# Performance work log

Measured on AMD Instinct MI355X. Metric: run time of the kernel, lower is better.

Reference implementation:

```python
import jax, jax.numpy as jnp
import numpy as np
from jax import lax

HEATMAP_THRESH = 0.1


def _conv(x, w, b, stride=1):
    y = lax.conv_general_dilated(x, w, (stride, stride), 'SAME',
                                 dimension_numbers=('NCHW', 'OIHW', 'NCHW'))
    return y + b[None, :, None, None]


def _maxpool2(x):
    return lax.reduce_window(x, -jnp.inf, lax.max, (1, 1, 2, 2), (1, 1, 2, 2), 'VALID')


def _up2(x):
    return jnp.repeat(jnp.repeat(x, 2, axis=2), 2, axis=3)


def _find_peaks_mask(hm, thresh):
    # Vectorized equivalent of the CPU nested-loop _find_peaks:
    # interior pixel is a peak iff v > thresh and v >= its 4 axial neighbors.
    c = hm[:, :, 1:-1, 1:-1]
    m = ((c > thresh)
         & (c >= hm[:, :, :-2, 1:-1]) & (c >= hm[:, :, 2:, 1:-1])
         & (c >= hm[:, :, 1:-1, :-2]) & (c >= hm[:, :, 1:-1, 2:]))
    return jnp.pad(m, ((0, 0), (0, 0), (1, 1), (1, 1)))  # border never a peak


def _param(key, shape):
    fan_in = int(np.prod(shape[1:]))
    return jax.random.normal(key, shape, jnp.float32) / np.sqrt(fan_in)


_SHAPES = {
    'w_d1': (32, 3, 3, 3), 'w_d2': (64, 32, 3, 3), 'w_bn': (128, 64, 3, 3),
    'w_u1': (64, 192, 3, 3), 'w_u2': (32, 96, 3, 3), 'w_seg': (1, 32, 1, 1),
    'w_p1': (64, 4, 3, 3), 'w_p2': (128, 64, 3, 3),
    'w_hm': (17, 128, 1, 1), 'w_paf': (32, 128, 1, 1),
}


def setup_inputs() -> dict:
    key = jax.random.key(0)
    ks = jax.random.split(key, 1 + len(_SHAPES))
    B, H, W = 8, 384, 384
    inp = {'x': jax.random.normal(ks[0], (B, 3, H, W), jnp.float32)}
    for i, (n, s) in enumerate(_SHAPES.items()):
        inp[n] = _param(ks[i + 1], s)
        inp[n.replace('w_', 'b_')] = jnp.zeros((s[0],), jnp.float32)
    return inp


def _forward(x, w_d1, b_d1, w_d2, b_d2, w_bn, b_bn, w_u1, b_u1, w_u2, b_u2,
             w_seg, b_seg, w_p1, b_p1, w_p2, b_p2, w_hm, b_hm, w_paf, b_paf):
    # --- UNet segmentation ---
    d1 = jax.nn.relu(_conv(x, w_d1, b_d1))                    # [B,32,384,384]
    d2 = jax.nn.relu(_conv(_maxpool2(d1), w_d2, b_d2))        # [B,64,192,192]
    bn = jax.nn.relu(_conv(_maxpool2(d2), w_bn, b_bn))        # [B,128,96,96]
    u1 = jax.nn.relu(_conv(jnp.concatenate([_up2(bn), d2], 1), w_u1, b_u1))  # [B,64,192,192]
    u2 = jax.nn.relu(_conv(jnp.concatenate([_up2(u1), d1], 1), w_u2, b_u2))  # [B,32,384,384]
    seg = _conv(u2, w_seg, b_seg)                             # [B,1,384,384]
    # --- Pose net on image + detached seg logits ---
    xp = jnp.concatenate([x, lax.stop_gradient(seg)], axis=1)  # detach()
    p1 = jax.nn.relu(_conv(xp, w_p1, b_p1, stride=2))          # [B,64,192,192]
    p2 = jax.nn.relu(_conv(p1, w_p2, b_p2, stride=2))          # [B,128,96,96]
    hm = _conv(p2, w_hm, b_hm)                                 # [B,17,96,96]
    paf = _conv(p2, w_paf, b_paf)                              # [B,32,96,96]
    return seg, hm, paf


def reference(x, w_d1, b_d1, w_d2, b_d2, w_bn, b_bn, w_u1, b_u1, w_u2, b_u2,
              w_seg, b_seg, w_p1, b_p1, w_p2, b_p2, w_hm, b_hm, w_paf, b_paf):
    seg, hm, paf = _forward(x, w_d1, b_d1, w_d2, b_d2, w_bn, b_bn, w_u1, b_u1,
                            w_u2, b_u2, w_seg, b_seg, w_p1, b_p1, w_p2, b_p2,
                            w_hm, b_hm, w_paf, b_paf)
    # jit-friendly replacement for the variable-length python peak lists:
    # boolean mask over [B,K,h,w]; (x,y) coords recoverable via jnp.nonzero offline.
    peaks = _find_peaks_mask(hm, HEATMAP_THRESH)
    return seg, hm, paf, peaks
```

## Files before the change

### kernel.cpp

```cpp
#include <hip/hip_runtime.h>


#define BS 256
#define BSW 512

typedef _Float16 half8 __attribute__((ext_vector_type(8)));
typedef float floatx4 __attribute__((ext_vector_type(4)));

#define LDSDW 20
#define PLT8 10000
#define ESTR 388

__global__ __launch_bounds__(BS) void packw_gen_kernel(
    const float* __restrict__ w, _Float16* __restrict__ bp, int Cin, int Cout)
{
    int total = (Cin >> 5) * 9 * (Cout >> 4) * 64;
    int tid = blockIdx.x * BS + threadIdx.x;
    if (tid >= total) return;
    int lane = tid & 63;
    int t = tid >> 6;
    int NTl = Cout >> 4;
    int nt = t % NTl; t /= NTl;
    int tap = t % 9;
    int chunk = t / 9;
    int q = lane >> 4, n = lane & 15;
    int co = nt * 16 + n;
    _Float16* ph = bp + (size_t)tid * 8;
    _Float16* pl = bp + (size_t)total * 8 + (size_t)tid * 8;
#pragma unroll
    for (int j = 0; j < 8; ++j) {
        int ci = chunk * 32 + q * 8 + j;
        float v = w[((size_t)co * Cin + ci) * 9 + tap];
        _Float16 h = (_Float16)v;
        ph[j] = h;
        pl[j] = (_Float16)(v - (float)h);
    }
}

__global__ __launch_bounds__(BS) void packw_1x1_kernel(
    const float* __restrict__ w, _Float16* __restrict__ bp, int Cin, int NTl, int Cout)
{
    int total = (Cin >> 5) * NTl * 64;
    int tid = blockIdx.x * BS + threadIdx.x;
    if (tid >= total) return;
    int lane = tid & 63;
    int t = tid >> 6;
    int nt = t % NTl;
    int chunk = t / NTl;
    int q = lane >> 4, n = lane & 15;
    int co = nt * 16 + n;
    _Float16* ph = bp + (size_t)tid * 8;
    _Float16* pl = bp + (size_t)total * 8 + (size_t)tid * 8;
#pragma unroll
    for (int j = 0; j < 8; ++j) {
        int ci = chunk * 32 + q * 8 + j;
        float v = (co < Cout) ? w[(size_t)co * Cin + ci] : 0.f;
        _Float16 h = (_Float16)v;
        ph[j] = h;
        pl[j] = (_Float16)(v - (float)h);
    }
}

template <int TCO>
__global__ __launch_bounds__(BS, 2) void conv3x3_pool_kernel(
    const float* __restrict__ inA, int Ca,
    const float* __restrict__ w, const float* __restrict__ b,
    _Float16* __restrict__ oph, _Float16* __restrict__ opl,
    int N, int H, int W, int Cout)
{
    const int W8 = W >> 3;
    const int H2 = H >> 1, W2 = W >> 1;
    int idx = blockIdx.x * BS + threadIdx.x;
    int total = N * H2 * W8;
    if (idx >= total) return;
    int x8 = idx % W8;
    int t  = idx / W8;
    int yo = t % H2;
    int n  = t / H2;
    int x0 = x8 << 3;
    const int co0 = blockIdx.y * TCO;
    const bool left_ok  = (x0 > 0);
    const bool right_ok = (x0 + 8 < W);
    const int Cin = Ca;

    float pool[TCO][4];

#pragma unroll
    for (int rr = 0; rr < 2; ++rr) {
        int y = 2 * yo + rr;
        float acc[TCO][8];
#pragma unroll
        for (int j = 0; j < TCO; ++j) {
            float bv = b[co0 + j];
#pragma unroll
            for (int p = 0; p < 8; ++p) acc[j][p] = bv;
        }

        for (int ci = 0; ci < Cin; ++ci) {
            float v[3][10];
#pragma unroll
            for (int ky = 0; ky < 3; ++ky) {
                int iy = y + ky - 1;
                if (iy < 0 || iy >= H) {
#pragma unroll
                    for (int p = 0; p < 10; ++p) v[ky][p] = 0.f;
                    continue;
                }
                const float* r = inA + ((size_t)(n * Ca + ci) * H + iy) * W;
                v[ky][0] = left_ok ? r[x0 - 1] : 0.f;
                float4 q0 = *(const float4*)(r + x0);
                float4 q1 = *(const float4*)(r + x0 + 4);
                v[ky][1] = q0.x; v[ky][2] = q0.y; v[ky][3] = q0.z; v[ky][4] = q0.w;
                v[ky][5] = q1.x; v[ky][6] = q1.y; v[ky][7] = q1.z; v[ky][8] = q1.w;
                v[ky][9] = right_ok ? r[x0 + 8] : 0.f;
            }
#pragma unroll
            for (int j = 0; j < TCO; ++j) {
                const float* wp = w + ((size_t)(co0 + j) * Cin + ci) * 9;
#pragma unroll
                for (int ky = 0; ky < 3; ++ky) {
                    float w0 = wp[ky * 3 + 0], w1 = wp[ky * 3 + 1], w2 = wp[ky * 3 + 2];
#pragma unroll
                    for (int p = 0; p < 8; ++p)
                        acc[j][p] += w0 * v[ky][p] + w1 * v[ky][p + 1] + w2 * v[ky][p + 2];
                }
            }
        }

#pragma unroll
        for (int j = 0; j < TCO; ++j) {
#pragma unroll
            for (int p4 = 0; p4 < 4; ++p4) {
                float mrow = fmaxf(fmaxf(acc[j][2 * p4], 0.f),
                                   fmaxf(acc[j][2 * p4 + 1], 0.f));
                pool[j][p4] = (rr == 0) ? mrow : fmaxf(pool[j][p4], mrow);
            }
        }
    }

#pragma unroll
    for (int p4 = 0; p4 < 4; ++p4) {
        half8 hv, lv;
#pragma unroll
        for (int j = 0; j < 8; ++j) {
            float v = pool[j][p4];
            _Float16 hh = (_Float16)v;
            hv[j] = hh;
            lv[j] = (_Float16)(v - (float)hh);
        }
        size_t oa = ((size_t)((n * (Cout >> 3) + (co0 >> 3)) * H2 + yo) * W2
                     + (x0 >> 1) + p4) * 8;
        *(half8*)(oph + oa) = hv;
        *(half8*)(opl + oa) = lv;
    }
}

template <int CHUNKS, int NT, int HH, int WW, int OUTMODE>
__global__ __launch_bounds__(BS) void conv3x3s_mfma_kernel(
    const _Float16* __restrict__ inh, const _Float16* __restrict__ inl,
    const _Float16* __restrict__ bp,
    const float* __restrict__ bias,
    float* __restrict__ out,
    _Float16* __restrict__ osph,
    _Float16* __restrict__ ospl,
    _Float16* __restrict__ oph,
    _Float16* __restrict__ opl)
{
    constexpr int PL = 4 * 34 * LDSDW;
    constexpr int EPI = 64 * NT * 16;
    constexpr int LDS_DW = (2 * PL > EPI) ? 2 * PL : EPI;
    __shared__ unsigned int lds[LDS_DW];

    int xblks = WW / 32;
    int b = blockIdx.x;
    int xb = b % xblks; b /= xblks;
    int yp = b % (HH / 2);
    int n  = b / (HH / 2);
    int y0 = yp * 2;
    int x0 = xb * 32;

    int tid = threadIdx.x;
    int lane = tid & 63, wv = tid >> 6;
    int m = lane & 15, q = lane >> 4;
    int lrow = wv >> 1;
    int lx   = (wv & 1) * 16;

    floatx4 acc[NT];
#pragma unroll
    for (int nt = 0; nt < NT; ++nt) acc[nt] = (floatx4){0.f, 0.f, 0.f, 0.f};

    const int planeW = CHUNKS * 9 * NT * 64 * 8;

    for (int chunk = 0; chunk < CHUNKS; ++chunk) {
        __syncthreads();
        for (int e = tid; e < 4 * 34 * 4; e += BS) {
            int xi = e % 34;
            int rest = e / 34;
            int oct = rest & 3;
            int row = rest >> 2;
            int iy = y0 - 1 + row, gx = x0 - 1 + xi;
            half8 hv = {}, lv = {};
            if (iy >= 0 && iy < HH && gx >= 0 && gx < WW) {
                size_t ga = ((size_t)((n * (CHUNKS * 4) + chunk * 4 + oct) * HH + iy) * WW + gx) * 8;
                hv = *(const half8*)(inh + ga);
                lv = *(const half8*)(inl + ga);
            }
            int base = (row * 34 + xi) * LDSDW + oct * 4;
            *(half8*)((char*)lds + (size_t)base * 4) = hv;
            *(half8*)((char*)lds + ((size_t)PL + base) * 4) = lv;
        }
        __syncthreads();
#pragma unroll
        for (int ky = 0; ky < 3; ++ky) {
#pragma unroll
            for (int kx = 0; kx < 3; ++kx) {
                int row = lrow + ky;
                int xi  = lx + m + kx;
                int adw = (row * 34 + xi) * LDSDW + q * 4;
                half8 ah = *(const half8*)((const char*)lds + (size_t)adw * 4);
                half8 al = *(const half8*)((const char*)lds + ((size_t)PL + adw) * 4);
                int tap = ky * 3 + kx;
                const _Float16* bpp = bp + ((size_t)(chunk * 9 + tap) * NT) * 64 * 8;
#pragma unroll
                for (int nt = 0; nt < NT; ++nt) {
                    half8 bh = *(const half8*)(bpp + ((size_t)nt * 64 + lane) * 8);
                    half8 bl = *(const half8*)(bpp + planeW + ((size_t)nt * 64 + lane) * 8);
                    acc[nt] = __builtin_amdgcn_mfma_f32_16x16x32_f16(ah, bh, acc[nt], 0, 0, 0);
                    acc[nt] = __builtin_amdgcn_mfma_f32_16x16x32_f16(ah, bl, acc[nt], 0, 0, 0);
                    acc[nt] = __builtin_amdgcn_mfma_f32_16x16x32_f16(al, bh, acc[nt], 0, 0, 0);
                }
            }
        }
    }

    __syncthreads();
#pragma unroll
    for (int nt = 0; nt < NT; ++nt) {
#pragma unroll
        for (int r = 0; r < 4; ++r) {
            int co = nt * 16 + m;
            int pxl = wv * 16 + q * 4 + r;
            ((float*)lds)[co * 64 + pxl] = acc[nt][r];
        }
    }
    __syncthreads();
    if (OUTMODE == 0 || OUTMODE == 2) {
        constexpr int thPerCo = 256 / (NT * 16);
        constexpr int pxPerTh = 64 / thPerCo;
        int co = tid / thPerCo;
        int sub = tid % thPerCo;
        int pxb = sub * pxPerTh;
        float bb = bias[co];
#pragma unroll
        for (int u = 0; u < pxPerTh; u += 4) {
            int p = pxb + u;
            int row = y0 + (p >> 5), xx = x0 + (p & 31);
            const float* lp = (const float*)lds + co * 64 + p;
            float4 vv = *(const float4*)lp;
            vv.x = fmaxf(vv.x + bb, 0.f);
            vv.y = fmaxf(vv.y + bb, 0.f);
            vv.z = fmaxf(vv.z + bb, 0.f);
            vv.w = fmaxf(vv.w + bb, 0.f);
            *(float4*)(out + ((size_t)(n * NT * 16 + co) * HH + row) * WW + xx) = vv;
        }
    }
    if (OUTMODE >= 1) {
        constexpr int OCTS = NT * 2;
        for (int it = tid; it < OCTS * 64; it += BS) {
            int px = it & 63;
            int oct = it >> 6;
            int row = y0 + (px >> 5), xx = x0 + (px & 31);
            half8 hv, lv;
#pragma unroll
            for (int j = 0; j < 8; ++j) {
                float v = fmaxf(((float*)lds)[(oct * 8 + j) * 64 + px] + bias[oct * 8 + j], 0.f);
                _Float16 hh = (_Float16)v;
                hv[j] = hh;
                lv[j] = (_Float16)(v - (float)hh);
            }
            size_t oaddr = ((size_t)((n * OCTS + oct) * HH + row) * WW + xx) * 8;
            *(half8*)(osph + oaddr) = hv;
            *(half8*)(ospl + oaddr) = lv;
        }
    }
    if (OUTMODE == 3) {
        constexpr int OCTS = NT * 2;
        constexpr int HHo = HH / 2, WWo = WW / 2;
        for (int it = tid; it < OCTS * 16; it += BS) {
            int xo = it & 15;
            int oct = it >> 4;
            half8 hv, lv;
#pragma unroll
            for (int j = 0; j < 8; ++j) {
                const float* base = (const float*)lds + (oct * 8 + j) * 64;
                float bb = bias[oct * 8 + j];
                float t0 = fmaxf(fmaxf(base[2 * xo] + bb, 0.f),
                                 fmaxf(base[2 * xo + 1] + bb, 0.f));
                float t1 = fmaxf(fmaxf(base[32 + 2 * xo] + bb, 0.f),
                                 fmaxf(base[32 + 2 * xo + 1] + bb, 0.f));
                float v = fmaxf(t0, t1);
                _Float16 hh = (_Float16)v;
                hv[j] = hh;
                lv[j] = (_Float16)(v - (float)hh);
            }
            size_t oaddr = ((size_t)((n * OCTS + oct) * HHo + yp) * WWo + (x0 >> 1) + xo) * 8;
            *(half8*)(oph + oaddr) = hv;
            *(half8*)(opl + oaddr) = lv;
        }
    }
}

template <int CHUNKS, int NT, int WI>
__global__ __launch_bounds__(BS) void conv3x3s2s_mfma_kernel(
    const _Float16* __restrict__ inh, const _Float16* __restrict__ inl,
    const _Float16* __restrict__ bp,
    const float* __restrict__ bias,
    _Float16* __restrict__ oh, _Float16* __restrict__ ol_)
{
    constexpr int WO = WI / 2;
    constexpr int PLs = 5 * 68 * LDSDW;
    constexpr int EPI = 64 * NT * 16;
    constexpr int LDS_DW = (2 * PLs > EPI) ? 2 * PLs : EPI;
    __shared__ unsigned int lds[LDS_DW];

    int xblks = WO / 32;
    int b = blockIdx.x;
    int xb = b % xblks; b /= xblks;
    int yp = b % (WO / 2);
    int n  = b / (WO / 2);
    int y0 = yp * 2;
    int x0 = xb * 32;

    int tid = threadIdx.x;
    int lane = tid & 63, wv = tid >> 6;
    int m = lane & 15, q = lane >> 4;
    int lrow = wv >> 1;
    int lx   = (wv & 1) * 16;

    floatx4 acc[NT];
#pragma unroll
    for (int nt = 0; nt < NT; ++nt) acc[nt] = (floatx4){0.f, 0.f, 0.f, 0.f};

    const int planeW = CHUNKS * 9 * NT * 64 * 8;

    for (int chunk = 0; chunk < CHUNKS; ++chunk) {
        __syncthreads();
        for (int e = tid; e < 5 * 68 * 4; e += BS) {
            int xi = e % 68;
            int rest = e / 68;
            int oct = rest & 3;
            int row = rest >> 2;
            int iy = 2 * y0 + row, ix = 2 * x0 + xi;
            half8 hv = {}, lv = {};
            if (xi < 65 && iy < WI && ix < WI) {
                size_t ga = ((size_t)((n * (CHUNKS * 4) + chunk * 4 + oct) * WI + iy) * WI + ix) * 8;
                hv = *(const half8*)(inh + ga);
                lv = *(const half8*)(inl + ga);
            }
            int pos = (xi & 1) * 34 + (xi >> 1);
            int base = (row * 68 + pos) * LDSDW + oct * 4;
            *(half8*)((char*)lds + (size_t)base * 4) = hv;
            *(half8*)((char*)lds + ((size_t)PLs + base) * 4) = lv;
        }
        __syncthreads();
#pragma unroll
        for (int ky = 0; ky < 3; ++ky) {
#pragma unroll
            for (int kx = 0; kx < 3; ++kx) {
                int row = 2 * lrow + ky;
                int pos = (kx & 1) * 34 + (lx + m) + (kx >> 1);
                int adw = (row * 68 + pos) * LDSDW + q * 4;
                half8 ah = *(const half8*)((const char*)lds + (size_t)adw * 4);
                half8 al = *(const half8*)((const char*)lds + ((size_t)PLs + adw) * 4);
                int tap = ky * 3 + kx;
                const _Float16* bpp = bp + ((size_t)(chunk * 9 + tap) * NT) * 64 * 8;
#pragma unroll
                for (int nt = 0; nt < NT; ++nt) {
                    half8 bh = *(const half8*)(bpp + ((size_t)nt * 64 + lane) * 8);
                    half8 bl = *(const half8*)(bpp + planeW + ((size_t)nt * 64 + lane) * 8);
                    acc[nt] = __builtin_amdgcn_mfma_f32_16x16x32_f16(ah, bh, acc[nt], 0, 0, 0);
                    acc[nt] = __builtin_amdgcn_mfma_f32_16x16x32_f16(ah, bl, acc[nt], 0, 0, 0);
                    acc[nt] = __builtin_amdgcn_mfma_f32_16x16x32_f16(al, bh, acc[nt], 0, 0, 0);
                }
            }
        }
    }

    __syncthreads();
#pragma unroll
    for (int nt = 0; nt < NT; ++nt) {
#pragma unroll
        for (int r = 0; r < 4; ++r) {
            int co = nt * 16 + m;
            int pxl = wv * 16 + q * 4 + r;
            ((float*)lds)[co * 64 + pxl] = acc[nt][r];
        }
    }
    __syncthreads();
    {
        constexpr int OCTS = NT * 2;
        for (int it = tid; it < OCTS * 64; it += BS) {
            int px = it & 63;
            int oct = it >> 6;
            int row = y0 + (px >> 5), xx = x0 + (px & 31);
            half8 hv, lv;
#pragma unroll
            for (int j = 0; j < 8; ++j) {
                float v = fmaxf(((float*)lds)[(oct * 8 + j) * 64 + px] + bias[oct * 8 + j], 0.f);
                _Float16 hh = (_Float16)v;
                hv[j] = hh;
                lv[j] = (_Float16)(v - (float)hh);
            }
            size_t oaddr = ((size_t)((n * OCTS + oct) * WO + row) * WO + xx) * 8;
            *(half8*)(oh + oaddr) = hv;
            *(half8*)(ol_ + oaddr) = lv;
        }
    }
}

template <int CHUNKS, int NT>
__global__ __launch_bounds__(BS) void conv1x1s_mfma_kernel(
    const _Float16* __restrict__ inh, const _Float16* __restrict__ inl,
    const _Float16* __restrict__ bp,
    const float* __restrict__ bias,
    float* __restrict__ out,
    int Cout, int HW)
{
    constexpr int PL1 = 64 * LDSDW;
    constexpr int EPI = 64 * NT * 16;
    constexpr int LDS_DW = (2 * PL1 > EPI) ? 2 * PL1 : EPI;
    __shared__ unsigned int lds[LDS_DW];

    int pblks = HW / 64;
    int b = blockIdx.x;
    int pb = b % pblks;
    int n  = b / pblks;
    int sp0 = pb * 64;

    int tid = threadIdx.x;
    int lane = tid & 63, wv = tid >> 6;
    int m = lane & 15, q = lane >> 4;

    floatx4 acc[NT];
#pragma unroll
    for (int nt = 0; nt < NT; ++nt) acc[nt] = (floatx4){0.f, 0.f, 0.f, 0.f};

    const int planeW = CHUNKS * NT * 64 * 8;

    for (int chunk = 0; chunk < CHUNKS; ++chunk) {
        __syncthreads();
        {
            int px = tid & 63;
            int oct = tid >> 6;
            size_t ga = (((size_t)(n * (CHUNKS * 4) + chunk * 4 + oct)) * HW + sp0 + px) * 8;
            half8 hv = *(const half8*)(inh + ga);
            half8 lv = *(const half8*)(inl + ga);
            int base = px * LDSDW + oct * 4;
            *(half8*)((char*)lds + (size_t)base * 4) = hv;
            *(half8*)((char*)lds + ((size_t)PL1 + base) * 4) = lv;
        }
        __syncthreads();
        {
            int adw = (wv * 16 + m) * LDSDW + q * 4;
            half8 ah = *(const half8*)((const char*)lds + (size_t)adw * 4);
            half8 al = *(const half8*)((const char*)lds + ((size_t)PL1 + adw) * 4);
            const _Float16* bpp = bp + ((size_t)chunk * NT) * 64 * 8;
#pragma unroll
            for (int nt = 0; nt < NT; ++nt) {
                half8 bh = *(const half8*)(bpp + ((size_t)nt * 64 + lane) * 8);
                half8 bl = *(const half8*)(bpp + planeW + ((size_t)nt * 64 + lane) * 8);
                acc[nt] = __builtin_amdgcn_mfma_f32_16x16x32_f16(ah, bh, acc[nt], 0, 0, 0);
                acc[nt] = __builtin_amdgcn_mfma_f32_16x16x32_f16(ah, bl, acc[nt], 0, 0, 0);
                acc[nt] = __builtin_amdgcn_mfma_f32_16x16x32_f16(al, bh, acc[nt], 0, 0, 0);
            }
        }
    }

    __syncthreads();
#pragma unroll
    for (int nt = 0; nt < NT; ++nt) {
#pragma unroll
        for (int r = 0; r < 4; ++r) {
            ((float*)lds)[(nt * 16 + m) * 64 + wv * 16 + q * 4 + r] = acc[nt][r];
        }
    }
    __syncthreads();
    {
        constexpr int thPerCo = 256 / (NT * 16);
        constexpr int pxPerTh = 64 / thPerCo;
        int co = tid / thPerCo;
        int g  = tid % thPerCo;
        if (co < Cout) {
            float bb = bias[co];
            const float* lp = (const float*)lds + co * 64 + g * pxPerTh;
            float* op = out + ((size_t)(n * Cout + co)) * HW + sp0 + g * pxPerTh;
#pragma unroll
            for (int u = 0; u < pxPerTh; u += 4) {
                float4 vv = *(const float4*)(lp + u);
                vv.x += bb; vv.y += bb; vv.z += bb; vv.w += bb;
                *(float4*)(op + u) = vv;
            }
        }
    }
}

__global__ __launch_bounds__(BSW) void u1_mfma_kernel(
    const _Float16* __restrict__ bnh, const _Float16* __restrict__ bnl,
    const _Float16* __restrict__ d2h, const _Float16* __restrict__ d2l,
    const _Float16* __restrict__ bp,
    const float* __restrict__ b_u1,
    _Float16* __restrict__ oh, _Float16* __restrict__ ol_)
{
    __shared__ unsigned int lds[2 * PLT8];
    const int Ho = 192, Wo = 192;
    int b = blockIdx.x;
    int xb = b % 4; b /= 4;
    int yb = b % 24;
    int n  = b / 24;
    int y0 = yb * 8;
    int x0 = xb * 48;

    int tid = threadIdx.x;
    int lane = tid & 63, wv = tid >> 6;
    int m = lane & 15, q = lane >> 4;
    int yr = y0 + wv;

    floatx4 acc[3][4];
#pragma unroll
    for (int mt = 0; mt < 3; ++mt)
#pragma unroll
        for (int nt = 0; nt < 4; ++nt) acc[mt][nt] = (floatx4){0.f, 0.f, 0.f, 0.f};

    const int hh0 = (y0 - 1) >> 1;
    const int hx0 = (x0 - 1) >> 1;

    for (int chunk = 0; chunk < 6; ++chunk) {
        __syncthreads();
        if (chunk < 4) {
            for (int e = tid; e < 6 * 26 * 4; e += BSW) {
                int xi = e % 26;
                int rest = e / 26;
                int oct = rest & 3;
                int row = rest >> 2;
                int hy = hh0 + row, hx = hx0 + xi;
                half8 hv = {}, lv = {};
                if (hy >= 0 && hy < 96 && hx >= 0 && hx < 96) {
                    size_t ga = ((size_t)((n * 16 + chunk * 4 + oct) * 96 + hy) * 96 + hx) * 8;
                    hv = *(const half8*)(bnh + ga);
                    lv = *(const half8*)(bnl + ga);
                }
                int base = (row * 50 + xi) * LDSDW + oct * 4;
                *(half8*)((char*)lds + (size_t)base * 4) = hv;
                *(half8*)((char*)lds + ((size_t)PLT8 + base) * 4) = lv;
            }
        } else {
            for (int e = tid; e < 10 * 50 * 4; e += BSW) {
                int xi = e % 50;
                int rest = e / 50;
                int oct = rest & 3;
                int row = rest >> 2;
                int iy = y0 - 1 + row, gx = x0 - 1 + xi;
                half8 hv = {}, lv = {};
                if (iy >= 0 && iy < Ho && gx >= 0 && gx < Wo) {
                    size_t ga = ((size_t)((n * 8 + (chunk - 4) * 4 + oct) * Ho + iy) * Wo + gx) * 8;
                    hv = *(const half8*)(d2h + ga);
                    lv = *(const half8*)(d2l + ga);
                }
                int base = (row * 50 + xi) * LDSDW + oct * 4;
                *(half8*)((char*)lds + (size_t)base * 4) = hv;
                *(half8*)((char*)lds + ((size_t)PLT8 + base) * 4) = lv;
            }
        }
        __syncthreads();
#pragma unroll
        for (int ky = 0; ky < 3; ++ky) {
#pragma unroll
            for (int kx = 0; kx < 3; ++kx) {
                int tap = ky * 3 + kx;
                const _Float16* bpp = bp + ((size_t)(chunk * 9 + tap) * 4) * 64 * 8;
                half8 bh[4], bl[4];
#pragma unroll
                for (int nt = 0; nt < 4; ++nt) {
                    bh[nt] = *(const half8*)(bpp + ((size_t)nt * 64 + lane) * 8);
                    bl[nt] = *(const half8*)(bpp + 110592 + ((size_t)nt * 64 + lane) * 8);
                }
                int row;
                if (chunk < 4) row = ((yr + ky - 1) >> 1) - hh0;
                else           row = wv + ky;
#pragma unroll
                for (int mt = 0; mt < 3; ++mt) {
                    int px = 16 * mt + m;
                    int xi = (chunk < 4) ? (((x0 + px + kx - 1) >> 1) - hx0)
                                         : (px + kx);
                    int adw = (row * 50 + xi) * LDSDW + q * 4;
                    half8 ah = *(const half8*)((const char*)lds + (size_t)adw * 4);
                    half8 al = *(const half8*)((const char*)lds + ((size_t)PLT8 + adw) * 4);
#pragma unroll
                    for (int nt = 0; nt < 4; ++nt) {
                        acc[mt][nt] = __builtin_amdgcn_mfma_f32_16x16x32_f16(ah, bh[nt], acc[mt][nt], 0, 0, 0);
                        acc[mt][nt] = __builtin_amdgcn_mfma_f32_16x16x32_f16(ah, bl[nt], acc[mt][nt], 0, 0, 0);
                        acc[mt][nt] = __builtin_amdgcn_mfma_f32_16x16x32_f16(al, bh[nt], acc[mt][nt], 0, 0, 0);
                    }
                }
            }
        }
    }

#pragma unroll
    for (int h = 0; h < 2; ++h) {
        __syncthreads();
#pragma unroll
        for (int ntl = 0; ntl < 2; ++ntl) {
#pragma unroll
            for (int mt = 0; mt < 3; ++mt) {
#pragma unroll
                for (int r = 0; r < 4; ++r) {
                    ((float*)lds)[(ntl * 16 + m) * ESTR + wv * 48 + 16 * mt + q * 4 + r]
                        = acc[mt][h * 2 + ntl][r];
                }
            }
        }
        __syncthreads();
        for (int it = tid; it < 4 * 384; it += BSW) {
            int px = it % 384;
            int ol = it / 384;
            int row = y0 + px / 48, xx = x0 + px % 48;
            half8 hv, lv;
#pragma unroll
            for (int j = 0; j < 8; ++j) {
                int col = ol * 8 + j;
                float v = fmaxf(((float*)lds)[col * ESTR + px] + b_u1[h * 32 + col], 0.f);
                _Float16 hh = (_Float16)v;
                hv[j] = hh;
                lv[j] = (_Float16)(v - (float)hh);
            }
            size_t oaddr = ((size_t)((n * 8 + h * 4 + ol) * Ho + row) * Wo + xx) * 8;
            *(half8*)(oh + oaddr) = hv;
            *(half8*)(ol_ + oaddr) = lv;
        }
    }
}

__global__ __launch_bounds__(BSW) void u2seg_mfma_kernel(
    const _Float16* __restrict__ u1h, const _Float16* __restrict__ u1l,
    const _Float16* __restrict__ d1h, const _Float16* __restrict__ d1l,
    const _Float16* __restrict__ bp,
    const float* __restrict__ b_u2,
    const float* __restrict__ w_seg,
    const float* __restrict__ b_seg,
    float* __restrict__ seg)
// ... 244 lines not shown
    int n  = t / Ho;
    int ox0 = q << 2;
    int ix0 = ox0 << 1;
    const int co0 = blockIdx.y * TCO;
    const bool right_ok = (ix0 + 8 < Wi);
    const int Cin = Ca + Cb;

    float acc[TCO][4];
#pragma unroll
    for (int j = 0; j < TCO; ++j) {
        float bv = b[co0 + j];
        acc[j][0] = bv; acc[j][1] = bv; acc[j][2] = bv; acc[j][3] = bv;
    }

    for (int ci = 0; ci < Cin; ++ci) {
        const float* base = (ci < Ca)
            ? inA + (size_t)(n * Ca + ci) * Hi * Wi
            : inB + (size_t)(n * Cb + (ci - Ca)) * Hi * Wi;
        float v[3][9];
#pragma unroll
        for (int ky = 0; ky < 3; ++ky) {
            int iy = 2 * oy + ky;
            if (iy >= Hi) {
#pragma unroll
                for (int p = 0; p < 9; ++p) v[ky][p] = 0.f;
                continue;
            }
            const float* r = base + (size_t)iy * Wi + ix0;
            float4 a = *(const float4*)r;
            float4 c = *(const float4*)(r + 4);
            v[ky][0] = a.x; v[ky][1] = a.y; v[ky][2] = a.z; v[ky][3] = a.w;
            v[ky][4] = c.x; v[ky][5] = c.y; v[ky][6] = c.z; v[ky][7] = c.w;
            v[ky][8] = right_ok ? r[8] : 0.f;
        }
#pragma unroll
        for (int j = 0; j < TCO; ++j) {
            const float* wp = w + ((size_t)(co0 + j) * Cin + ci) * 9;
#pragma unroll
            for (int ky = 0; ky < 3; ++ky) {
                float w0 = wp[ky * 3 + 0], w1 = wp[ky * 3 + 1], w2 = wp[ky * 3 + 2];
#pragma unroll
                for (int p = 0; p < 4; ++p)
                    acc[j][p] += w0 * v[ky][2 * p] + w1 * v[ky][2 * p + 1] + w2 * v[ky][2 * p + 2];
            }
        }
    }

    if (SPLIT) {
#pragma unroll
        for (int p = 0; p < 4; ++p) {
            half8 hv, lv;
#pragma unroll
            for (int j = 0; j < 8; ++j) {
                float v = acc[j][p];
                if (do_relu) v = fmaxf(v, 0.f);
                _Float16 hh = (_Float16)v;
                hv[j] = hh;
                lv[j] = (_Float16)(v - (float)hh);
            }
            size_t oaddr = ((size_t)((n * (Cout >> 3) + (co0 >> 3)) * Ho + oy) * Wo + ox0 + p) * 8;
            *(half8*)(osph + oaddr) = hv;
            *(half8*)(ospl + oaddr) = lv;
        }
    } else {
#pragma unroll
        for (int j = 0; j < TCO; ++j) {
            float4 o;
            o.x = acc[j][0]; o.y = acc[j][1]; o.z = acc[j][2]; o.w = acc[j][3];
            if (do_relu) {
                o.x = fmaxf(o.x, 0.f); o.y = fmaxf(o.y, 0.f);
                o.z = fmaxf(o.z, 0.f); o.w = fmaxf(o.w, 0.f);
            }
            *(float4*)(out + ((size_t)(n * Cout + co0 + j) * Ho + oy) * Wo + ox0) = o;
        }
    }
}

__global__ __launch_bounds__(BS) void peaks_kernel(
    const float* __restrict__ hm, float* __restrict__ out,
    int NC, int H, int W, float thresh)
{
    int idx = blockIdx.x * BS + threadIdx.x;
    int total = NC * H * W;
    if (idx >= total) return;
    int x = idx % W;
    int t = idx / W;
    int y = t % H;
    int c = t / H;
    float r = 0.f;
    if (x >= 1 && x < W - 1 && y >= 1 && y < H - 1) {
        const float* base = hm + (size_t)c * H * W;
        float cv = base[y * W + x];
        if (cv > thresh &&
            cv >= base[(y - 1) * W + x] &&
            cv >= base[(y + 1) * W + x] &&
            cv >= base[y * W + (x - 1)] &&
            cv >= base[y * W + (x + 1)])
            r = 1.f;
    }
    out[idx] = r;
}

static inline int nblk(long n) { return (int)((n + BS - 1) / BS); }

extern "C" void kernel_launch(void* const* d_in, const int* in_sizes, int n_in,
                              void* d_out, int out_size, void* d_ws, size_t ws_size,
                              hipStream_t stream)
{
    const float* x     = (const float*)d_in[0];
    const float* w_d1  = (const float*)d_in[1];  const float* b_d1  = (const float*)d_in[2];
    const float* w_d2  = (const float*)d_in[3];  const float* b_d2  = (const float*)d_in[4];
    const float* w_bn  = (const float*)d_in[5];  const float* b_bn  = (const float*)d_in[6];
    const float* w_u1  = (const float*)d_in[7];  const float* b_u1  = (const float*)d_in[8];
    const float* w_u2  = (const float*)d_in[9];  const float* b_u2  = (const float*)d_in[10];
    const float* w_seg = (const float*)d_in[11]; const float* b_seg = (const float*)d_in[12];
    const float* w_p1  = (const float*)d_in[13]; const float* b_p1  = (const float*)d_in[14];
    const float* w_p2  = (const float*)d_in[15]; const float* b_p2  = (const float*)d_in[16];
    const float* w_hm  = (const float*)d_in[17]; const float* b_hm  = (const float*)d_in[18];
    const float* w_paf = (const float*)d_in[19]; const float* b_paf = (const float*)d_in[20];

    const int N = 8, H = 384, W = 384;
    const int H2 = 192, W2 = 192, H4 = 96, W4 = 96;

    float* ws = (float*)d_ws;
    _Float16* pd1sp_h = (_Float16*)(ws);
    _Float16* pd1sp_l = (_Float16*)(ws + 4718592);
    _Float16* d2sp_h = (_Float16*)(ws + 28311552);
    _Float16* d2sp_l = (_Float16*)(ws + 37748736);
    _Float16* pd2sp_h = (_Float16*)(ws + 47185920);
    _Float16* pd2sp_l = (_Float16*)(ws + 49545216);
    _Float16* bnsp_h = (_Float16*)(ws + 18874368);
    _Float16* bnsp_l = (_Float16*)(ws + 23592960);
    _Float16* u1sp_h = (_Float16*)(ws);
    _Float16* u1sp_l = (_Float16*)(ws + 9437184);
    _Float16* d1sp_h = (_Float16*)(ws + 18874368);
    _Float16* d1sp_l = (_Float16*)(ws + 37748736);
    _Float16* p1sp_h = (_Float16*)(ws);
    _Float16* p1sp_l = (_Float16*)(ws + 9437184);
    _Float16* p2sp_h = (_Float16*)(ws + 18874368);
    _Float16* p2sp_l = (_Float16*)(ws + 23592960);

    float* out_seg   = (float*)d_out;
    float* out_hm    = out_seg + 1179648;
    float* out_paf   = out_hm + 1253376;
    float* out_peaks = out_paf + 2359296;
    _Float16* bp_u1  = (_Float16*)(out_seg + 4792320);
    _Float16* bp_u2  = (_Float16*)(out_seg + 4902912);
    _Float16* bp_d2  = (_Float16*)(out_seg + 4930560);
    _Float16* bp_bn  = (_Float16*)(out_seg + 4948992);
    _Float16* bp_p2  = (_Float16*)(out_seg + 5022720);
    _Float16* bp_hm  = (_Float16*)(out_seg + 5096448);
    _Float16* bp_paf = (_Float16*)(out_seg + 5100544);

    packw_gen_kernel<<<nblk(13824), BS, 0, stream>>>(w_u1, bp_u1, 192, 64);
    packw_gen_kernel<<<nblk(3456),  BS, 0, stream>>>(w_u2, bp_u2, 96, 32);
    packw_gen_kernel<<<nblk(2304),  BS, 0, stream>>>(w_d2, bp_d2, 32, 64);
    packw_gen_kernel<<<nblk(9216),  BS, 0, stream>>>(w_bn, bp_bn, 64, 128);
    packw_gen_kernel<<<nblk(9216),  BS, 0, stream>>>(w_p2, bp_p2, 64, 128);
    packw_1x1_kernel<<<nblk(512),   BS, 0, stream>>>(w_hm, bp_hm, 128, 2, 17);
    packw_1x1_kernel<<<nblk(512),   BS, 0, stream>>>(w_paf, bp_paf, 128, 2, 32);
    {
        dim3 g(nblk((long)N * H2 * (W / 8)), 32 / 8);
        conv3x3_pool_kernel<8><<<g, BS, 0, stream>>>(
            x, 3, w_d1, b_d1, pd1sp_h, pd1sp_l, N, H, W, 32);
    }
    conv3x3s_mfma_kernel<1, 4, 192, 192, 3><<<8 * 96 * 6, BS, 0, stream>>>(
        pd1sp_h, pd1sp_l, bp_d2, b_d2, nullptr, d2sp_h, d2sp_l, pd2sp_h, pd2sp_l);
    conv3x3s_mfma_kernel<2, 8, 96, 96, 1><<<8 * 48 * 3, BS, 0, stream>>>(
        pd2sp_h, pd2sp_l, bp_bn, b_bn, nullptr, bnsp_h, bnsp_l, nullptr, nullptr);
    u1_mfma_kernel<<<8 * 24 * 4, BSW, 0, stream>>>(
        bnsp_h, bnsp_l, d2sp_h, d2sp_l, bp_u1, b_u1, u1sp_h, u1sp_l);
    {
        dim3 g(nblk((long)N * H * (W / 8)), 32 / 8);
        conv3x3_x8_kernel<1, 8, 1><<<g, BS, 0, stream>>>(
            x, 3, nullptr, 0, w_d1, b_d1, nullptr, N, H, W, 32, 1, d1sp_h, d1sp_l);
    }
    u2seg_mfma_kernel<<<8 * 48 * 8, BSW, 0, stream>>>(
        u1sp_h, u1sp_l, d1sp_h, d1sp_l, bp_u2, b_u2, w_seg, b_seg, out_seg);
    {
        dim3 g(nblk((long)N * H2 * (W2 / 4)), 64 / 8);
        conv3x3_s2_co_kernel<8, 1><<<g, BS, 0, stream>>>(
            x, 3, out_seg, 1, w_p1, b_p1, nullptr, N, H, W, 64, 1, p1sp_h, p1sp_l);
    }
    conv3x3s2s_mfma_kernel<2, 8, 192><<<8 * 48 * 3, BS, 0, stream>>>(
        p1sp_h, p1sp_l, bp_p2, b_p2, p2sp_h, p2sp_l);
    conv1x1s_mfma_kernel<4, 2><<<8 * 144, BS, 0, stream>>>(
        p2sp_h, p2sp_l, bp_hm, b_hm, out_hm, 17, H4 * W4);
    conv1x1s_mfma_kernel<4, 2><<<8 * 144, BS, 0, stream>>>(
        p2sp_h, p2sp_l, bp_paf, b_paf, out_paf, 32, H4 * W4);
    peaks_kernel<<<nblk((long)N * 17 * H4 * W4), BS, 0, stream>>>(
        out_hm, out_peaks, N * 17, H4, W4, 0.1f);
}
```

Before: 906.5 us.

## Merge weight-pack launches, fuse 1x1 heads, retile d2 conv to 8-row blocks

Replaces seven weight-packing launches with one combined kernel, and fuses the heatmap and PAF 1x1 convolutions into a single kernel that reads p2 once. Adds a dedicated d2 conv kernel using 512-thread blocks over 8x48 tiles with 3x4 MFMA accumulators, which also writes the pooled output. The goal is to cut launch overhead, avoid reading p2 twice, and improve reuse of LDS input and weights. The cost is higher register pressure and a two-pass epilogue in the new d2 kernel.

```diff
diff --git a/kernel.cpp b/kernel.cpp
--- a/kernel.cpp
+++ b/kernel.cpp
@@ -11,12 +11,10 @@
 #define PLT8 10000
 #define ESTR 388
 
-__global__ __launch_bounds__(BS) void packw_gen_kernel(
-    const float* __restrict__ w, _Float16* __restrict__ bp, int Cin, int Cout)
-{
-    int total = (Cin >> 5) * 9 * (Cout >> 4) * 64;
-    int tid = blockIdx.x * BS + threadIdx.x;
-    if (tid >= total) return;
+__device__ inline void packw_gen_body(
+    const float* __restrict__ w, _Float16* __restrict__ bp, int Cin, int Cout,
+    int tid, int total)
+{
     int lane = tid & 63;
     int t = tid >> 6;
     int NTl = Cout >> 4;
@@ -37,12 +35,10 @@
     }
 }
 
-__global__ __launch_bounds__(BS) void packw_1x1_kernel(
-    const float* __restrict__ w, _Float16* __restrict__ bp, int Cin, int NTl, int Cout)
-{
-    int total = (Cin >> 5) * NTl * 64;
-    int tid = blockIdx.x * BS + threadIdx.x;
-    if (tid >= total) return;
+__device__ inline void packw_1x1_body(
+    const float* __restrict__ w, _Float16* __restrict__ bp, int Cin, int NTl, int Cout,
+    int tid, int total)
+{
     int lane = tid & 63;
     int t = tid >> 6;
     int nt = t % NTl;
@@ -59,6 +55,32 @@
         ph[j] = h;
         pl[j] = (_Float16)(v - (float)h);
     }
+}
+
+__global__ __launch_bounds__(BS) void packw_all_kernel(
+    const float* __restrict__ w_u1, const float* __restrict__ w_u2,
+    const float* __restrict__ w_d2, const float* __restrict__ w_bn,
+    const float* __restrict__ w_p2, const float* __restrict__ w_hm,
+    const float* __restrict__ w_paf,
+    _Float16* __restrict__ bp_u1, _Float16* __restrict__ bp_u2,
+    _Float16* __restrict__ bp_d2, _Float16* __restrict__ bp_bn,
+    _Float16* __restrict__ bp_p2, _Float16* __restrict__ bp_hm,
+    _Float16* __restrict__ bp_paf)
+{
+    int tid = blockIdx.x * BS + threadIdx.x;
+    if (tid < 13824) { packw_gen_body(w_u1, bp_u1, 192, 64, tid, 13824); return; }
+    tid -= 13824;
+    if (tid < 3456)  { packw_gen_body(w_u2, bp_u2, 96, 32, tid, 3456); return; }
+    tid -= 3456;
+    if (tid < 2304)  { packw_gen_body(w_d2, bp_d2, 32, 64, tid, 2304); return; }
+    tid -= 2304;
+    if (tid < 9216)  { packw_gen_body(w_bn, bp_bn, 64, 128, tid, 9216); return; }
+    tid -= 9216;
+    if (tid < 9216)  { packw_gen_body(w_p2, bp_p2, 64, 128, tid, 9216); return; }
+    tid -= 9216;
+    if (tid < 512)   { packw_1x1_body(w_hm, bp_hm, 128, 2, 17, tid, 512); return; }
+    tid -= 512;
+    if (tid < 512)   { packw_1x1_body(w_paf, bp_paf, 128, 2, 32, tid, 512); return; }
 }
 
 template <int TCO>
@@ -160,11 +182,8 @@
     const _Float16* __restrict__ inh, const _Float16* __restrict__ inl,
     const _Float16* __restrict__ bp,
     const float* __restrict__ bias,
-    float* __restrict__ out,
     _Float16* __restrict__ osph,
-    _Float16* __restrict__ ospl,
-    _Float16* __restrict__ oph,
-    _Float16* __restrict__ opl)
+    _Float16* __restrict__ ospl)
 {
     constexpr int PL = 4 * 34 * LDSDW;
     constexpr int EPI = 64 * NT * 16;
@@ -244,27 +263,7 @@
         }
     }
     __syncthreads();
-    if (OUTMODE == 0 || OUTMODE == 2) {
-        constexpr int thPerCo = 256 / (NT * 16);
-        constexpr int pxPerTh = 64 / thPerCo;
-        int co = tid / thPerCo;
-        int sub = tid % thPerCo;
-        int pxb = sub * pxPerTh;
-        float bb = bias[co];
-#pragma unroll
-        for (int u = 0; u < pxPerTh; u += 4) {
-            int p = pxb + u;
-            int row = y0 + (p >> 5), xx = x0 + (p & 31);
-            const float* lp = (const float*)lds + co * 64 + p;
-            float4 vv = *(const float4*)lp;
-            vv.x = fmaxf(vv.x + bb, 0.f);
-            vv.y = fmaxf(vv.y + bb, 0.f);
-            vv.z = fmaxf(vv.z + bb, 0.f);
-            vv.w = fmaxf(vv.w + bb, 0.f);
-            *(float4*)(out + ((size_t)(n * NT * 16 + co) * HH + row) * WW + xx) = vv;
-        }
-    }
-    if (OUTMODE >= 1) {
+    {
         constexpr int OCTS = NT * 2;
         for (int it = tid; it < OCTS * 64; it += BS) {
             int px = it & 63;
@@ -283,27 +282,135 @@
             *(half8*)(ospl + oaddr) = lv;
         }
     }
-    if (OUTMODE == 3) {
-        constexpr int OCTS = NT * 2;
-        constexpr int HHo = HH / 2, WWo = WW / 2;
-        for (int it = tid; it < OCTS * 16; it += BS) {
-            int xo = it & 15;
-            int oct = it >> 4;
+}
+
+__global__ __launch_bounds__(BSW) void d2_mfma8_kernel(
+    const _Float16* __restrict__ inh, const _Float16* __restrict__ inl,
+    const _Float16* __restrict__ bp,
+    const float* __restrict__ bias,
+    _Float16* __restrict__ oh, _Float16* __restrict__ ol_,
+    _Float16* __restrict__ oph, _Float16* __restrict__ opl)
+{
+    __shared__ unsigned int lds[2 * PLT8];
+    const int Ho = 192, Wo = 192;
+    int b = blockIdx.x;
+    int xb = b % 4; b /= 4;
+    int yb = b % 24;
+    int n  = b / 24;
+    int y0 = yb * 8;
+    int x0 = xb * 48;
+
+    int tid = threadIdx.x;
+    int lane = tid & 63, wv = tid >> 6;
+    int m = lane & 15, q = lane >> 4;
+
+    floatx4 acc[3][4];
+#pragma unroll
+    for (int mt = 0; mt < 3; ++mt)
+#pragma unroll
+        for (int nt = 0; nt < 4; ++nt) acc[mt][nt] = (floatx4){0.f, 0.f, 0.f, 0.f};
+
+    for (int e = tid; e < 10 * 50 * 4; e += BSW) {
+        int xi = e % 50;
+        int rest = e / 50;
+        int oct = rest & 3;
+        int row = rest >> 2;
+        int iy = y0 - 1 + row, gx = x0 - 1 + xi;
+        half8 hv = {}, lv = {};
+        if (iy >= 0 && iy < Ho && gx >= 0 && gx < Wo) {
+            size_t ga = ((size_t)((n * 4 + oct) * Ho + iy) * Wo + gx) * 8;
+            hv = *(const half8*)(inh + ga);
+            lv = *(const half8*)(inl + ga);
+        }
+        int base = (row * 50 + xi) * LDSDW + oct * 4;
+        *(half8*)((char*)lds + (size_t)base * 4) = hv;
+        *(half8*)((char*)lds + ((size_t)PLT8 + base) * 4) = lv;
+    }
+    __syncthreads();
+#pragma unroll
+    for (int ky = 0; ky < 3; ++ky) {
+#pragma unroll
+        for (int kx = 0; kx < 3; ++kx) {
+            int tap = ky * 3 + kx;
+            const _Float16* bpp = bp + (size_t)tap * 2048;
+            half8 bh[4], bl[4];
+#pragma unroll
+            for (int nt = 0; nt < 4; ++nt) {
+                bh[nt] = *(const half8*)(bpp + ((size_t)nt * 64 + lane) * 8);
+                bl[nt] = *(const half8*)(bpp + 18432 + ((size_t)nt * 64 + lane) * 8);
+            }
+            int row = wv + ky;
+#pragma unroll
+            for (int mt = 0; mt < 3; ++mt) {
+                int px = 16 * mt + m;
+                int xi = px + kx;
+                int adw = (row * 50 + xi) * LDSDW + q * 4;
+                half8 ah = *(const half8*)((const char*)lds + (size_t)adw * 4);
+                half8 al = *(const half8*)((const char*)lds + ((size_t)PLT8 + adw) * 4);
+#pragma unroll
+                for (int nt = 0; nt < 4; ++nt) {
+                    acc[mt][nt] = __builtin_amdgcn_mfma_f32_16x16x32_f16(ah, bh[nt], acc[mt][nt], 0, 0, 0);
+                    acc[mt][nt] = __builtin_amdgcn_mfma_f32_16x16x32_f16(ah, bl[nt], acc[mt][nt], 0, 0, 0);
+                    acc[mt][nt] = __builtin_amdgcn_mfma_f32_16x16x32_f16(al, bh[nt], acc[mt][nt], 0, 0, 0);
+                }
+            }
+        }
+    }
+
+#pragma unroll
+    for (int h = 0; h < 2; ++h) {
+        __syncthreads();
+#pragma unroll
+        for (int ntl = 0; ntl < 2; ++ntl) {
+#pragma unroll
+            for (int mt = 0; mt < 3; ++mt) {
+#pragma unroll
+                for (int r = 0; r < 4; ++r) {
+                    ((float*)lds)[(ntl * 16 + m) * ESTR + wv * 48 + 16 * mt + q * 4 + r]
+                        = acc[mt][h * 2 + ntl][r];
+                }
+            }
+        }
+        __syncthreads();
+        for (int it = tid; it < 4 * 384; it += BSW) {
+            int px = it % 384;
+            int ol = it / 384;
+            int row = y0 + px / 48, xx = x0 + px % 48;
             half8 hv, lv;
 #pragma unroll
             for (int j = 0; j < 8; ++j) {
-                const float* base = (const float*)lds + (oct * 8 + j) * 64;
-                float bb = bias[oct * 8 + j];
-                float t0 = fmaxf(fmaxf(base[2 * xo] + bb, 0.f),
-                                 fmaxf(base[2 * xo + 1] + bb, 0.f));
-                float t1 = fmaxf(fmaxf(base[32 + 2 * xo] + bb, 0.f),
-                                 fmaxf(base[32 + 2 * xo + 1] + bb, 0.f));
+                int col = ol * 8 + j;
+                float v = fmaxf(((float*)lds)[col * ESTR + px] + bias[h * 32 + col], 0.f);
+                _Float16 hh = (_Float16)v;
+                hv[j] = hh;
+                lv[j] = (_Float16)(v - (float)hh);
+            }
+            size_t oaddr = ((size_t)((n * 8 + h * 4 + ol) * Ho + row) * Wo + xx) * 8;
+            *(half8*)(oh + oaddr) = hv;
+            *(half8*)(ol_ + oaddr) = lv;
+        }
+        for (int it = tid; it < 4 * 4 * 24; it += BSW) {
+            int xo = it % 24;
+            int rest = it / 24;
+            int ro = rest & 3;
+            int ol = rest >> 2;
+            half8 hv, lv;
+#pragma unroll
+            for (int j = 0; j < 8; ++j) {
+                int col = ol * 8 + j;
+                float bb = bias[h * 32 + col];
+                const float* buf = (const float*)lds + col * ESTR;
+                float t0 = fmaxf(fmaxf(buf[(2 * ro) * 48 + 2 * xo] + bb, 0.f),
+                                 fmaxf(buf[(2 * ro) * 48 + 2 * xo + 1] + bb, 0.f));
+                float t1 = fmaxf(fmaxf(buf[(2 * ro + 1) * 48 + 2 * xo] + bb, 0.f),
+                                 fmaxf(buf[(2 * ro + 1) * 48 + 2 * xo + 1] + bb, 0.f));
                 float v = fmaxf(t0, t1);
                 _Float16 hh = (_Float16)v;
                 hv[j] = hh;
                 lv[j] = (_Float16)(v - (float)hh);
             }
-            size_t oaddr = ((size_t)((n * OCTS + oct) * HHo + yp) * WWo + (x0 >> 1) + xo) * 8;
+            size_t oaddr = ((size_t)((n * 8 + h * 4 + ol) * 96 + (yb * 4 + ro)) * 96
+                            + (xb * 24 + xo)) * 8;
             *(half8*)(oph + oaddr) = hv;
             *(half8*)(opl + oaddr) = lv;
         }
@@ -418,18 +525,14 @@
     }
 }
 
-template <int CHUNKS, int NT>
-__global__ __launch_bounds__(BS) void conv1x1s_mfma_kernel(
+__global__ __launch_bounds__(BS) void conv1x1_heads_kernel(
     const _Float16* __restrict__ inh, const _Float16* __restrict__ inl,
-    const _Float16* __restrict__ bp,
-    const float* __restrict__ bias,
-    float* __restrict__ out,
-    int Cout, int HW)
+    const _Float16* __restrict__ bph, const _Float16* __restrict__ bpp,
+    const float* __restrict__ bh_, const float* __restrict__ bpf,
+    float* __restrict__ out_hm, float* __restrict__ out_paf, int HW)
 {
     constexpr int PL1 = 64 * LDSDW;
-    constexpr int EPI = 64 * NT * 16;
-    constexpr int LDS_DW = (2 * PL1 > EPI) ? 2 * PL1 : EPI;
-    __shared__ unsigned int lds[LDS_DW];
+    __shared__ unsigned int lds[64 * 64];
 
     int pblks = HW / 64;
     int b = blockIdx.x;
@@ -441,18 +544,16 @@
     int lane = tid & 63, wv = tid >> 6;
     int m = lane & 15, q = lane >> 4;
 
-    floatx4 acc[NT];
-#pragma unroll
-    for (int nt = 0; nt < NT; ++nt) acc[nt] = (floatx4){0.f, 0.f, 0.f, 0.f};
-
-    const int planeW = CHUNKS * NT * 64 * 8;
-
-    for (int chunk = 0; chunk < CHUNKS; ++chunk) {
+    floatx4 acc[4];
+#pragma unroll
+    for (int nt = 0; nt < 4; ++nt) acc[nt] = (floatx4){0.f, 0.f, 0.f, 0.f};
+
+    for (int chunk = 0; chunk < 4; ++chunk) {
         __syncthreads();
         {
             int px = tid & 63;
             int oct = tid >> 6;
-            size_t ga = (((size_t)(n * (CHUNKS * 4) + chunk * 4 + oct)) * HW + sp0 + px) * 8;
+            size_t ga = (((size_t)(n * 16 + chunk * 4 + oct)) * HW + sp0 + px) * 8;
             half8 hv = *(const half8*)(inh + ga);
             half8 lv = *(const half8*)(inl + ga);
             int base = px * LDSDW + oct * 4;
@@ -464,11 +565,13 @@
             int adw = (wv * 16 + m) * LDSDW + q * 4;
             half8 ah = *(const half8*)((const char*)lds + (size_t)adw * 4);
             half8 al = *(const half8*)((const char*)lds + ((size_t)PL1 + adw) * 4);
-            const _Float16* bpp = bp + ((size_t)chunk * NT) * 64 * 8;
-#pragma unroll
-            for (int nt = 0; nt < NT; ++nt) {
-                half8 bh = *(const half8*)(bpp + ((size_t)nt * 64 + lane) * 8);
-                half8 bl = *(const half8*)(bpp + planeW + ((size_t)nt * 64 + lane) * 8);
+#pragma unroll
+            for (int nt = 0; nt < 4; ++nt) {
+                const _Float16* base = (nt < 2) ? bph : bpp;
+                int ntl = nt & 1;
+                const _Float16* pbh = base + (size_t)(chunk * 2 + ntl) * 512 + (size_t)lane * 8;
+                half8 bh = *(const half8*)pbh;
+                half8 bl = *(const half8*)(pbh + 4096);
                 acc[nt] = __builtin_amdgcn_mfma_f32_16x16x32_f16(ah, bh, acc[nt], 0, 0, 0);
                 acc[nt] = __builtin_amdgcn_mfma_f32_16x16x32_f16(ah, bl, acc[nt], 0, 0, 0);
                 acc[nt] = __builtin_amdgcn_mfma_f32_16x16x32_f16(al, bh, acc[nt], 0, 0, 0);
@@ -478,7 +581,7 @@
 
     __syncthreads();
 #pragma unroll
-    for (int nt = 0; nt < NT; ++nt) {
+    for (int nt = 0; nt < 4; ++nt) {
 #pragma unroll
         for (int r = 0; r < 4; ++r) {
             ((float*)lds)[(nt * 16 + m) * 64 + wv * 16 + q * 4 + r] = acc[nt][r];
@@ -486,16 +589,24 @@
     }
     __syncthreads();
     {
-        constexpr int thPerCo = 256 / (NT * 16);
-        constexpr int pxPerTh = 64 / thPerCo;
-        int co = tid / thPerCo;
-        int g  = tid % thPerCo;
-        if (co < Cout) {
-            float bb = bias[co];
-            const float* lp = (const float*)lds + co * 64 + g * pxPerTh;
-            float* op = out + ((size_t)(n * Cout + co)) * HW + sp0 + g * pxPerTh;
-#pragma unroll
-            for (int u = 0; u < pxPerTh; u += 4) {
+        int co = tid >> 2;
+        int g  = tid & 3;
+        const float* lp = (const float*)lds + co * 64 + g * 16;
+        if (co < 17) {
+            float bb = bh_[co];
+            float* op = out_hm + ((size_t)(n * 17 + co)) * HW + sp0 + g * 16;
+#pragma unroll
+            for (int u = 0; u < 16; u += 4) {
+                float4 vv = *(const float4*)(lp + u);
+                vv.x += bb; vv.y += bb; vv.z += bb; vv.w += bb;
+                *(float4*)(op + u) = vv;
+            }
+        } else if (co >= 32) {
+            int pco = co - 32;
+            float bb = bpf[pco];
+            float* op = out_paf + ((size_t)(n * 32 + pco)) * HW + sp0 + g * 16;
+#pragma unroll
+            for (int u = 0; u < 16; u += 4) {
                 float4 vv = *(const float4*)(lp + u);
                 vv.x += bb; vv.y += bb; vv.z += bb; vv.w += bb;
                 *(float4*)(op + u) = vv;
@@ -1046,22 +1157,18 @@
     _Float16* bp_hm  = (_Float16*)(out_seg + 5096448);
     _Float16* bp_paf = (_Float16*)(out_seg + 5100544);
 
-    packw_gen_kernel<<<nblk(13824), BS, 0, stream>>>(w_u1, bp_u1, 192, 64);
-    packw_gen_kernel<<<nblk(3456),  BS, 0, stream>>>(w_u2, bp_u2, 96, 32);
-    packw_gen_kernel<<<nblk(2304),  BS, 0, stream>>>(w_d2, bp_d2, 32, 64);
-    packw_gen_kernel<<<nblk(9216),  BS, 0, stream>>>(w_bn, bp_bn, 64, 128);
-    packw_gen_kernel<<<nblk(9216),  BS, 0, stream>>>(w_p2, bp_p2, 64, 128);
-    packw_1x1_kernel<<<nblk(512),   BS, 0, stream>>>(w_hm, bp_hm, 128, 2, 17);
-    packw_1x1_kernel<<<nblk(512),   BS, 0, stream>>>(w_paf, bp_paf, 128, 2, 32);
+    packw_all_kernel<<<nblk(39040), BS, 0, stream>>>(
+        w_u1, w_u2, w_d2, w_bn, w_p2, w_hm, w_paf,
+        bp_u1, bp_u2, bp_d2, bp_bn, bp_p2, bp_hm, bp_paf);
     {
         dim3 g(nblk((long)N * H2 * (W / 8)), 32 / 8);
         conv3x3_pool_kernel<8><<<g, BS, 0, stream>>>(
             x, 3, w_d1, b_d1, pd1sp_h, pd1sp_l, N, H, W, 32);
     }
-    conv3x3s_mfma_kernel<1, 4, 192, 192, 3><<<8 * 96 * 6, BS, 0, stream>>>(
-        pd1sp_h, pd1sp_l, bp_d2, b_d2, nullptr, d2sp_h, d2sp_l, pd2sp_h, pd2sp_l);
+    d2_mfma8_kernel<<<8 * 24 * 4, BSW, 0, stream>>>(
+        pd1sp_h, pd1sp_l, bp_d2, b_d2, d2sp_h, d2sp_l, pd2sp_h, pd2sp_l);
     conv3x3s_mfma_kernel<2, 8, 96, 96, 1><<<8 * 48 * 3, BS, 0, stream>>>(
-        pd2sp_h, pd2sp_l, bp_bn, b_bn, nullptr, bnsp_h, bnsp_l, nullptr, nullptr);
+        pd2sp_h, pd2sp_l, bp_bn, b_bn, bnsp_h, bnsp_l);
     u1_mfma_kernel<<<8 * 24 * 4, BSW, 0, stream>>>(
         bnsp_h, bnsp_l, d2sp_h, d2sp_l, bp_u1, b_u1, u1sp_h, u1sp_l);
     {
@@ -1078,10 +1185,8 @@
     }
     conv3x3s2s_mfma_kernel<2, 8, 192><<<8 * 48 * 3, BS, 0, stream>>>(
         p1sp_h, p1sp_l, bp_p2, b_p2, p2sp_h, p2sp_l);
-    conv1x1s_mfma_kernel<4, 2><<<8 * 144, BS, 0, stream>>>(
-        p2sp_h, p2sp_l, bp_hm, b_hm, out_hm, 17, H4 * W4);
-    conv1x1s_mfma_kernel<4, 2><<<8 * 144, BS, 0, stream>>>(
-        p2sp_h, p2sp_l, bp_paf, b_paf, out_paf, 32, H4 * W4);
+    conv1x1_heads_kernel<<<8 * 144, BS, 0, stream>>>(
+        p2sp_h, p2sp_l, bp_hm, bp_paf, b_hm, b_paf, out_hm, out_paf, H4 * W4);
     peaks_kernel<<<nblk((long)N * 17 * H4 * W4), BS, 0, stream>>>(
         out_hm, out_peaks, N * 17, H4, W4, 0.1f);
 }
```

Result: no change. 896.8 us (-1.1%).
